# Kernel optimization log

Hardware: AMD Instinct MI355X
Metric: run time of the kernel (lower is better)

## Reference

```python
import jax, jax.numpy as jnp
import numpy as np


def setup_inputs() -> dict:
    key = jax.random.key(0)
    ks = jax.random.split(key, 6)
    B, T, S, E, D = 8, 128, 512, 512, 512  # batch, trg_len, src_len, enc_dim, trg_dim
    W_SCALE = 0.03  # small init to keep tanh unsaturated
    return {
        "hidden": jax.random.normal(ks[0], (B, T, D), jnp.float32),
        "encoder_outputs": jax.random.normal(ks[1], (B, S, E), jnp.float32),
        "encoder_mask": jnp.ones((B, S), jnp.float32),
        "W_attn": jax.random.normal(ks[2], (D, E + D), jnp.float32) * W_SCALE,
        "b_attn": jnp.zeros((D,), jnp.float32),
        "W_v": jax.random.normal(ks[3], (1, D), jnp.float32) * W_SCALE,
        "b_v": jnp.zeros((1,), jnp.float32),
        "W_out": jax.random.normal(ks[4], (D, E + D), jnp.float32) * W_SCALE,
    }


def masked_softmax(x, m, axis=-1):
    # faithful to repo: x*m, stable exp, e*m, normalize with eps
    x = x * m
    e_x = jnp.exp(x - jnp.max(x, axis=axis, keepdims=True))
    e_x = e_x * m
    return e_x / (jnp.sum(e_x, axis=axis, keepdims=True) + 1e-6)


def reference(hidden, encoder_outputs, encoder_mask, W_attn, b_attn, W_v, b_v, W_out):
    B, T, D = hidden.shape
    S = encoder_outputs.shape[1]
    # concat order in get_energy is (hidden_i, encoder_outputs), so split W_attn
    W_h = W_attn[:, :D]   # (D_out, trg_dim)
    W_e = W_attn[:, D:]   # (D_out, enc_dim)
    # Linear(concat) == h@W_h^T + e@W_e^T + b; vectorized over all (t, s) pairs
    hp = jnp.einsum('btd,kd->btk', hidden, W_h)            # (B,T,K)
    ep = jnp.einsum('bse,ke->bsk', encoder_outputs, W_e)   # (B,S,K)
    feat = jnp.tanh(hp[:, :, None, :] + ep[:, None, :, :] + b_attn)  # (B,T,S,K)
    energies = jnp.einsum('btsk,k->bts', feat, W_v[0]) + b_v[0]      # (B,T,S)
    # forward: energies * mask, then masked softmax
    m = encoder_mask[:, None, :]  # (B,1,S)
    energies = energies * m
    attn_weights = masked_softmax(energies, m, axis=-1)    # (B,T,S)
    weighted_context = jnp.einsum('bts,bse->bte', attn_weights, encoder_outputs)
    h_cat = jnp.concatenate([weighted_context, hidden], axis=-1)  # (B,T,E+D)
    h_tilde = jnp.tanh(jnp.einsum('btc,dc->btd', h_cat, W_out))   # (B,T,D)
    return h_tilde, weighted_context, attn_weights
```

## Files before the change

### kernel.cpp

```cpp
#include <hip/hip_runtime.h>
#include <hip/hip_bf16.h>
#include <math.h>

typedef unsigned short u16;
typedef unsigned int u32;
typedef __bf16 bf16x8 __attribute__((ext_vector_type(8)));
typedef float f32x4 __attribute__((ext_vector_type(4)));

#define OUT_WC   524288LL
#define OUT_ATTN 1048576LL
#define C2 2.8853900817779268f
#define LOG2E 1.4426950408889634f
#define LAS 40

__device__ inline u16 f2b(float f) {
    return (u16)((__float_as_uint(f) + 0x8000u) >> 16);
}
__device__ inline float b2f(u16 v) { return __uint_as_float(((u32)v) << 16); }
__device__ inline u32 pkcvt(float x, float y) {
    __hip_bfloat162 h = __float22bfloat162_rn(make_float2(x, y));
    return *(u32*)&h;
}
__device__ inline float tanh_fast(float x) {
    return 1.f - 2.f * __builtin_amdgcn_rcpf(__builtin_amdgcn_exp2f(C2 * x) + 1.f);
}

__global__ __launch_bounds__(256) void tobf(
    const float* __restrict__ enc, const float* __restrict__ hidden,
    const float* __restrict__ Wattn, const float* __restrict__ Wout,
    u16* __restrict__ dst)
{
    long long i = ((long long)blockIdx.x * 256 + threadIdx.x) * 8;
    const float* src; long long off;
    if (i < 2097152)      { src = enc;    off = i; }
    else if (i < 2621440) { src = hidden; off = i - 2097152; }
    else if (i < 3145728) { src = Wattn;  off = i - 2621440; }
    else                  { src = Wout;   off = i - 3145728; }
    float4 v0 = *(const float4*)(src + off);
    float4 v1 = *(const float4*)(src + off + 4);
    *(uint4*)(dst + i) = make_uint4(pkcvt(v0.x, v0.y), pkcvt(v0.z, v0.w),
                                    pkcvt(v1.x, v1.y), pkcvt(v1.z, v1.w));
}

__global__ __launch_bounds__(256) void proj(
    const u16* __restrict__ hidden_bf, const u16* __restrict__ enc_bf,
    const u16* __restrict__ Wattn_bf, const float* __restrict__ battn,
    const u16* __restrict__ Wout_bf,
    float* __restrict__ hp, u16* __restrict__ ept, float* __restrict__ hh)
{
    __shared__ u16 lA[64 * LAS];
    __shared__ u16 lB[64 * LAS];
    const int tid = threadIdx.x;
    const int wvi = tid >> 6, ln = tid & 63;
    const int wm = wvi >> 1, wn = wvi & 1;
    const int l16 = ln & 15, quad = ln >> 4;
    const int blk = blockIdx.x;
    int bx, by, zz = 0, lda, ldb, mode;
    const u16 *A, *B;
    if (blk < 512) {
        mode = 0;
        zz = blk >> 6; by = (blk >> 3) & 7; bx = blk & 7;
        A = Wattn_bf + 512; lda = 1024;
        B = enc_bf + (long long)zz * 262144; ldb = 512;
    } else if (blk < 640) {
        mode = 1;
        int i = blk - 512; by = i >> 3; bx = i & 7;
        A = hidden_bf; lda = 512;
        B = Wattn_bf; ldb = 1024;
    } else {
        mode = 2;
        int i = blk - 640; by = i >> 3; bx = i & 7;
        A = hidden_bf; lda = 512;
        B = Wout_bf + 512; ldb = 1024;
    }
    const int m0 = by * 64, n0 = bx * 64;
    const int srow = tid >> 2, skof = (tid & 3) * 8;
    const u16* Ap = A + (long long)(m0 + srow) * lda + skof;
    const u16* Bp = B + (long long)(n0 + srow) * ldb + skof;

    f32x4 acc00 = {0,0,0,0}, acc01 = {0,0,0,0}, acc10 = {0,0,0,0}, acc11 = {0,0,0,0};

    for (int k0 = 0; k0 < 512; k0 += 32) {
        uint4 av = *(const uint4*)(Ap + k0);
        uint4 bv = *(const uint4*)(Bp + k0);
        __syncthreads();
        *(uint4*)&lA[srow * LAS + skof] = av;
        *(uint4*)&lB[srow * LAS + skof] = bv;
        __syncthreads();
        bf16x8 a0 = *(const bf16x8*)&lA[(wm * 32      + l16) * LAS + quad * 8];
        bf16x8 a1 = *(const bf16x8*)&lA[(wm * 32 + 16 + l16) * LAS + quad * 8];
        bf16x8 b0 = *(const bf16x8*)&lB[(wn * 32      + l16) * LAS + quad * 8];
        bf16x8 b1 = *(const bf16x8*)&lB[(wn * 32 + 16 + l16) * LAS + quad * 8];
        acc00 = __builtin_amdgcn_mfma_f32_16x16x32_bf16(a0, b0, acc00, 0, 0, 0);
        acc01 = __builtin_amdgcn_mfma_f32_16x16x32_bf16(a0, b1, acc01, 0, 0, 0);
        acc10 = __builtin_amdgcn_mfma_f32_16x16x32_bf16(a1, b0, acc10, 0, 0, 0);
        acc11 = __builtin_amdgcn_mfma_f32_16x16x32_bf16(a1, b1, acc11, 0, 0, 0);
    }

    const f32x4* accs[4] = { &acc00, &acc01, &acc10, &acc11 };
    #pragma unroll
    for (int i = 0; i < 2; ++i) {
        #pragma unroll
        for (int j = 0; j < 2; ++j) {
            const f32x4& a = *accs[i * 2 + j];
            #pragma unroll
            for (int r = 0; r < 4; ++r) {
                int m = m0 + wm * 32 + i * 16 + quad * 4 + r;
                int n = n0 + wn * 32 + j * 16 + l16;
                float v = a[r];
                if (mode == 0)
                    ept[(long long)zz * 262144 + (long long)m * 512 + n] =
                        f2b(__builtin_amdgcn_exp2f(C2 * v));
                else if (mode == 1)
                    hp[(long long)m * 512 + n] = C2 * (v + battn[n]);
                else
                    hh[(long long)m * 512 + n] = v;
            }
        }
    }
}

__device__ inline float wred_sum(float v) {
    #pragma unroll
    for (int i = 32; i > 0; i >>= 1) v += __shfl_xor(v, i);
    return v;
}
__device__ inline float bred_sum8(float v, float* red, int tid) {
    v = wred_sum(v);
    __syncthreads();
    if ((tid & 63) == 0) red[tid >> 6] = v;
    __syncthreads();
    float s = 0.f;
    #pragma unroll
    for (int i = 0; i < 8; ++i) s += red[i];
    return s;
}
__device__ inline void bred2_max(float v0, float v1, float* red, int tid,
                                 float* o0, float* o1) {
    #pragma unroll
    for (int i = 32; i > 0; i >>= 1) {
        v0 = fmaxf(v0, __shfl_xor(v0, i));
        v1 = fmaxf(v1, __shfl_xor(v1, i));
    }
    __syncthreads();
    if ((tid & 63) == 0) { red[tid >> 6] = v0; red[8 + (tid >> 6)] = v1; }
    __syncthreads();
    float a0 = red[0], a1 = red[8];
    #pragma unroll
    for (int i = 1; i < 8; ++i) { a0 = fmaxf(a0, red[i]); a1 = fmaxf(a1, red[8 + i]); }
    *o0 = a0; *o1 = a1;
}
__device__ inline void bred2_sum(float v0, float v1, float* red, int tid,
                                 float* o0, float* o1) {
    #pragma unroll
    for (int i = 32; i > 0; i >>= 1) { v0 += __shfl_xor(v0, i); v1 += __shfl_xor(v1, i); }
    __syncthreads();
    if ((tid & 63) == 0) { red[tid >> 6] = v0; red[8 + (tid >> 6)] = v1; }
    __syncthreads();
    float a0 = 0.f, a1 = 0.f;
    #pragma unroll
    for (int i = 0; i < 8; ++i) { a0 += red[i]; a1 += red[8 + i]; }
    *o0 = a0; *o1 = a1;
}

__device__ inline void proc8(uint4 c, float4 hw, float* a0, float* a1) {
    u32 cc[4] = {c.x, c.y, c.z, c.w};
    #pragma unroll
    for (int i = 0; i < 4; ++i) {
        float xl = __uint_as_float(cc[i] << 16);
        float xh = __uint_as_float(cc[i] & 0xFFFF0000u);
        float rl0 = __builtin_amdgcn_rcpf(fmaf(hw.x, xl, 1.f));
        float rh0 = __builtin_amdgcn_rcpf(fmaf(hw.x, xh, 1.f));
        float rl1 = __builtin_amdgcn_rcpf(fmaf(hw.y, xl, 1.f));
        float rh1 = __builtin_amdgcn_rcpf(fmaf(hw.y, xh, 1.f));
        a0[2*i]   = fmaf(hw.z, rl0, a0[2*i]);
        a0[2*i+1] = fmaf(hw.z, rh0, a0[2*i+1]);
        a1[2*i]   = fmaf(hw.z, rl1, a1[2*i]);
        a1[2*i+1] = fmaf(hw.z, rh1, a1[2*i+1]);
    }
}

__global__ __launch_bounds__(512) void energies(
    const float* __restrict__ maskp, const float* __restrict__ hp,
    const u16* __restrict__ ept, const float* __restrict__ Wv,
    const float* __restrict__ bvp, const u16* __restrict__ enc_bf,
    float* __restrict__ attn, float* __restrict__ wc)
{
    __shared__ __align__(16) float4 hpw[512];
    __shared__ float pa[2][8][512];
    __shared__ __align__(16) float2 aL[512];
    __shared__ float red[16];
    const int tid = threadIdx.x;
    const int b = blockIdx.x >> 6;
    const int t0 = (blockIdx.x & 63) * 2;

    float w = Wv[tid];
    float h0 = hp[(long long)(b * 128 + t0) * 512 + tid];
    float h1 = hp[(long long)(b * 128 + t0 + 1) * 512 + tid];
    hpw[tid] = make_float4(__builtin_amdgcn_exp2f(h0), __builtin_amdgcn_exp2f(h1), w, 0.f);
    float sumWv = bred_sum8(w, red, tid);

    const int kg = tid >> 6, sl = tid & 63;
    const int s0 = sl * 8;
    const u16* eb = ept + (long long)b * 262144 + (kg * 64) * 512 + s0;
    const float4* hq = &hpw[kg * 64];

    float a0[8] = {0,0,0,0,0,0,0,0}, a1[8] = {0,0,0,0,0,0,0,0};
    uint4 c0 = *(const uint4*)(eb);
    uint4 c1 = *(const uint4*)(eb + 512);
    uint4 c2 = *(const uint4*)(eb + 1024);
    uint4 c3 = *(const uint4*)(eb + 1536);
    for (int kk = 0; kk < 60; kk += 4) {
        const u16* nb = eb + (kk + 4) * 512;
        uint4 n0 = *(const uint4*)(nb);
        uint4 n1 = *(const uint4*)(nb + 512);
        uint4 n2 = *(const uint4*)(nb + 1024);
        uint4 n3 = *(const uint4*)(nb + 1536);
        proc8(c0, hq[kk],     a0, a1);
        proc8(c1, hq[kk + 1], a0, a1);
        proc8(c2, hq[kk + 2], a0, a1);
        proc8(c3, hq[kk + 3], a0, a1);
        c0 = n0; c1 = n1; c2 = n2; c3 = n3;
    }
    proc8(c0, hq[60], a0, a1);
    proc8(c1, hq[61], a0, a1);
    proc8(c2, hq[62], a0, a1);
    proc8(c3, hq[63], a0, a1);

    *(float4*)&pa[0][kg][s0]     = make_float4(a0[0], a0[1], a0[2], a0[3]);
    *(float4*)&pa[0][kg][s0 + 4] = make_float4(a0[4], a0[5], a0[6], a0[7]);
    *(float4*)&pa[1][kg][s0]     = make_float4(a1[0], a1[1], a1[2], a1[3]);
    *(float4*)&pa[1][kg][s0 + 4] = make_float4(a1[4], a1[5], a1[6], a1[7]);
    __syncthreads();

    const int s = tid;
    float A0 = 0.f, A1 = 0.f;
    #pragma unroll
    for (int g = 0; g < 8; ++g) { A0 += pa[0][g][s]; A1 += pa[1][g][s]; }
    float mv = maskp[(long long)b * 512 + s];
    float bv0 = bvp[0];
    float r0 = (bv0 + sumWv - 2.f * A0) * mv; r0 *= mv;
    float r1 = (bv0 + sumWv - 2.f * A1) * mv; r1 *= mv;

    float mx0, mx1;
    bred2_max(r0, r1, red, tid, &mx0, &mx1);
    float ex0 = __builtin_amdgcn_exp2f((r0 - mx0) * LOG2E) * mv;
    float ex1 = __builtin_amdgcn_exp2f((r1 - mx1) * LOG2E) * mv;
    float sm0, sm1;
    bred2_sum(ex0, ex1, red, tid, &sm0, &sm1);
    float at0 = ex0 * (1.f / (sm0 + 1e-6f));
    float at1 = ex1 * (1.f / (sm1 + 1e-6f));
    attn[(long long)(b * 128 + t0) * 512 + s]     = at0;
    attn[(long long)(b * 128 + t0 + 1) * 512 + s] = at1;
    aL[s] = make_float2(at0, at1);
    __syncthreads();

    const u16* encb = enc_bf + (long long)b * 262144 + tid;
    const float4* aL4 = (const float4*)aL;
    float acc0 = 0.f, acc1 = 0.f;
    for (int ss = 0; ss < 512; ss += 8) {
        float ev[8];
        #pragma unroll
        for (int i = 0; i < 8; ++i) ev[i] = b2f(encb[(ss + i) * 512]);
        #pragma unroll
        for (int i = 0; i < 4; ++i) {
            float4 ap = aL4[(ss >> 1) + i];
            acc0 = fmaf(ap.x, ev[2*i],   acc0);
            acc1 = fmaf(ap.y, ev[2*i],   acc1);
            acc0 = fmaf(ap.z, ev[2*i+1], acc0);
            acc1 = fmaf(ap.w, ev[2*i+1], acc1);
        }
    }
    wc[(long long)(b * 128 + t0) * 512 + tid]     = acc0;
    wc[(long long)(b * 128 + t0 + 1) * 512 + tid] = acc1;
}

__global__ __launch_bounds__(256) void hout_k(
    const float* __restrict__ wc, const u16* __restrict__ Wout_bf,
    float* __restrict__ out)
{
    __shared__ u16 lA[32 * LAS];
    __shared__ u16 lB[64 * LAS];
    const int tid = threadIdx.x;
    const int wvi = tid >> 6, ln = tid & 63;
    const int l16 = ln & 15, quad = ln >> 4;
    const int msub = wvi & 1, npair = wvi >> 1;
    const int m0 = blockIdx.y * 32, n0 = blockIdx.x * 64;
    const int rowA = tid >> 3, kofA = (tid & 7) * 4;
    const int rowB = tid >> 2, kofB = (tid & 3) * 8;
    f32x4 acc0 = {0,0,0,0}, acc1 = {0,0,0,0};

    for (int k0 = 0; k0 < 512; k0 += 32) {
        float4 av = *(const float4*)(wc + (long long)(m0 + rowA) * 512 + k0 + kofA);
        uint4 bv = *(const uint4*)(Wout_bf + (long long)(n0 + rowB) * 1024 + k0 + kofB);
        __syncthreads();
        *(uint2*)&lA[rowA * LAS + kofA] = make_uint2(pkcvt(av.x, av.y), pkcvt(av.z, av.w));
        int kk = kofB ^ (((rowB >> 3) & 3) << 3);
        *(uint4*)&lB[rowB * LAS + kk] = bv;
        __syncthreads();
        bf16x8 a = *(const bf16x8*)&lA[(msub * 16 + l16) * LAS + quad * 8];
        int nr0 = npair * 32 + l16, nr1 = nr0 + 16;
        bf16x8 b0 = *(const bf16x8*)&lB[nr0 * LAS + (quad * 8 ^ (((nr0 >> 3) & 3) << 3))];
        bf16x8 b1 = *(const bf16x8*)&lB[nr1 * LAS + (quad * 8 ^ (((nr1 >> 3) & 3) << 3))];
        acc0 = __builtin_amdgcn_mfma_f32_16x16x32_bf16(a, b0, acc0, 0, 0, 0);
        acc1 = __builtin_amdgcn_mfma_f32_16x16x32_bf16(a, b1, acc1, 0, 0, 0);
    }
    #pragma unroll
    for (int j = 0; j < 2; ++j) {
        const f32x4& a = j ? acc1 : acc0;
        #pragma unroll
        for (int r = 0; r < 4; ++r) {
            int m = m0 + msub * 16 + quad * 4 + r;
            int n = n0 + npair * 32 + j * 16 + l16;
            long long idx = (long long)m * 512 + n;
            out[idx] = tanh_fast(a[r] + out[idx]);
        }
    }
}

extern "C" void kernel_launch(void* const* d_in, const int* in_sizes, int n_in,
                              void* d_out, int out_size, void* d_ws, size_t ws_size,
                              hipStream_t stream)
{
    const float* hidden = (const float*)d_in[0];
    const float* enc    = (const float*)d_in[1];
    const float* mask   = (const float*)d_in[2];
    const float* Wattn  = (const float*)d_in[3];
    const float* battn  = (const float*)d_in[4];
    const float* Wv     = (const float*)d_in[5];
    const float* bvp    = (const float*)d_in[6];
    const float* Wout   = (const float*)d_in[7];
    float* out = (float*)d_out;

    float* hp  = (float*)d_ws;
    u16*   ept = (u16*)((char*)d_ws + (2 << 20));
    u16*   bfp = (u16*)((char*)d_ws + (6 << 20));
    u16* enc_bf    = bfp;
    u16* hidden_bf = bfp + 2097152;
    u16* Wattn_bf  = bfp + 2621440;
    u16* Wout_bf   = bfp + 3145728;

    tobf<<<1792, 256, 0, stream>>>(enc, hidden, Wattn, Wout, bfp);
    proj<<<768, 256, 0, stream>>>(hidden_bf, enc_bf, Wattn_bf, battn, Wout_bf,
                                  hp, ept, out );
    energies<<<512, 512, 0, stream>>>(mask, hp, ept, Wv, bvp, enc_bf,
                                      out + OUT_ATTN, out + OUT_WC);
    hout_k<<<dim3(8, 32, 1), 256, 0, stream>>>(out + OUT_WC, Wout_bf, out);
}
```

Before: 148.9 us.

## Enlarge proj GEMM tiles to 128x128 with register prefetch of next K slice

The projection GEMM kernel now computes 128x128 output tiles per block instead of 64x64, with each wave holding a 4x4 grid of MFMA accumulators, and it loads the next K slice into registers while the current slice is being consumed. The larger tiles raise data reuse per LDS load and cut global traffic, and the prefetch is meant to hide global load latency. The trade-off is that the grid shrinks from 768 to 192 blocks, which is fewer than the CU count on MI355X, and register pressure per thread goes up. The LDS row padding also changes to 36.

```diff
diff --git a/kernel.cpp b/kernel.cpp
--- a/kernel.cpp
+++ b/kernel.cpp
@@ -12,6 +12,7 @@
 #define C2 2.8853900817779268f
 #define LOG2E 1.4426950408889634f
 #define LAS 40
+#define PLAS 36
 
 __device__ inline u16 f2b(float f) {
     return (u16)((__float_as_uint(f) + 0x8000u) >> 16);
@@ -48,66 +49,79 @@
     const u16* __restrict__ Wout_bf,
     float* __restrict__ hp, u16* __restrict__ ept, float* __restrict__ hh)
 {
-    __shared__ u16 lA[64 * LAS];
-    __shared__ u16 lB[64 * LAS];
+    __shared__ u16 lA[128 * PLAS];
+    __shared__ u16 lB[128 * PLAS];
     const int tid = threadIdx.x;
     const int wvi = tid >> 6, ln = tid & 63;
     const int wm = wvi >> 1, wn = wvi & 1;
     const int l16 = ln & 15, quad = ln >> 4;
     const int blk = blockIdx.x;
-    int bx, by, zz = 0, lda, ldb, mode;
+    int mode, bx, by, zz = 0, lda, ldb;
     const u16 *A, *B;
-    if (blk < 512) {
+    if (blk < 128) {
         mode = 0;
-        zz = blk >> 6; by = (blk >> 3) & 7; bx = blk & 7;
+        zz = blk >> 4; by = (blk >> 2) & 3; bx = blk & 3;
         A = Wattn_bf + 512; lda = 1024;
         B = enc_bf + (long long)zz * 262144; ldb = 512;
-    } else if (blk < 640) {
+    } else if (blk < 160) {
         mode = 1;
-        int i = blk - 512; by = i >> 3; bx = i & 7;
+        int i = blk - 128; by = i >> 2; bx = i & 3;
         A = hidden_bf; lda = 512;
         B = Wattn_bf; ldb = 1024;
     } else {
         mode = 2;
-        int i = blk - 640; by = i >> 3; bx = i & 7;
+        int i = blk - 160; by = i >> 2; bx = i & 3;
         A = hidden_bf; lda = 512;
         B = Wout_bf + 512; ldb = 1024;
     }
-    const int m0 = by * 64, n0 = bx * 64;
-    const int srow = tid >> 2, skof = (tid & 3) * 8;
-    const u16* Ap = A + (long long)(m0 + srow) * lda + skof;
-    const u16* Bp = B + (long long)(n0 + srow) * ldb + skof;
-
-    f32x4 acc00 = {0,0,0,0}, acc01 = {0,0,0,0}, acc10 = {0,0,0,0}, acc11 = {0,0,0,0};
+    const int m0 = by * 128, n0 = bx * 128;
+    const int sr = tid >> 2, sc = (tid & 3) * 8;
+    const u16* Ap0 = A + (long long)(m0 + sr) * lda + sc;
+    const u16* Ap1 = A + (long long)(m0 + sr + 64) * lda + sc;
+    const u16* Bp0 = B + (long long)(n0 + sr) * ldb + sc;
+    const u16* Bp1 = B + (long long)(n0 + sr + 64) * ldb + sc;
+
+    f32x4 acc[4][4] = {};
+    uint4 ra0 = *(const uint4*)(Ap0);
+    uint4 ra1 = *(const uint4*)(Ap1);
+    uint4 rb0 = *(const uint4*)(Bp0);
+    uint4 rb1 = *(const uint4*)(Bp1);
 
     for (int k0 = 0; k0 < 512; k0 += 32) {
-        uint4 av = *(const uint4*)(Ap + k0);
-        uint4 bv = *(const uint4*)(Bp + k0);
         __syncthreads();
-        *(uint4*)&lA[srow * LAS + skof] = av;
-        *(uint4*)&lB[srow * LAS + skof] = bv;
+        *(uint4*)&lA[sr * PLAS + sc]        = ra0;
+        *(uint4*)&lA[(sr + 64) * PLAS + sc] = ra1;
+        *(uint4*)&lB[sr * PLAS + sc]        = rb0;
+        *(uint4*)&lB[(sr + 64) * PLAS + sc] = rb1;
         __syncthreads();
-        bf16x8 a0 = *(const bf16x8*)&lA[(wm * 32      + l16) * LAS + quad * 8];
-        bf16x8 a1 = *(const bf16x8*)&lA[(wm * 32 + 16 + l16) * LAS + quad * 8];
-        bf16x8 b0 = *(const bf16x8*)&lB[(wn * 32      + l16) * LAS + quad * 8];
-        bf16x8 b1 = *(const bf16x8*)&lB[(wn * 32 + 16 + l16) * LAS + quad * 8];
-        acc00 = __builtin_amdgcn_mfma_f32_16x16x32_bf16(a0, b0, acc00, 0, 0, 0);
-        acc01 = __builtin_amdgcn_mfma_f32_16x16x32_bf16(a0, b1, acc01, 0, 0, 0);
-        acc10 = __builtin_amdgcn_mfma_f32_16x16x32_bf16(a1, b0, acc10, 0, 0, 0);
-        acc11 = __builtin_amdgcn_mfma_f32_16x16x32_bf16(a1, b1, acc11, 0, 0, 0);
-    }
-
-    const f32x4* accs[4] = { &acc00, &acc01, &acc10, &acc11 };
-    #pragma unroll
-    for (int i = 0; i < 2; ++i) {
-        #pragma unroll
-        for (int j = 0; j < 2; ++j) {
-            const f32x4& a = *accs[i * 2 + j];
+        if (k0 + 32 < 512) {
+            ra0 = *(const uint4*)(Ap0 + k0 + 32);
+            ra1 = *(const uint4*)(Ap1 + k0 + 32);
+            rb0 = *(const uint4*)(Bp0 + k0 + 32);
+            rb1 = *(const uint4*)(Bp1 + k0 + 32);
+        }
+        bf16x8 af[4], bfr[4];
+        #pragma unroll
+        for (int i = 0; i < 4; ++i) {
+            af[i]  = *(const bf16x8*)&lA[(wm * 64 + i * 16 + l16) * PLAS + quad * 8];
+            bfr[i] = *(const bf16x8*)&lB[(wn * 64 + i * 16 + l16) * PLAS + quad * 8];
+        }
+        #pragma unroll
+        for (int i = 0; i < 4; ++i)
+            #pragma unroll
+            for (int j = 0; j < 4; ++j)
+                acc[i][j] = __builtin_amdgcn_mfma_f32_16x16x32_bf16(af[i], bfr[j], acc[i][j], 0, 0, 0);
+    }
+
+    #pragma unroll
+    for (int i = 0; i < 4; ++i) {
+        #pragma unroll
+        for (int j = 0; j < 4; ++j) {
             #pragma unroll
             for (int r = 0; r < 4; ++r) {
-                int m = m0 + wm * 32 + i * 16 + quad * 4 + r;
-                int n = n0 + wn * 32 + j * 16 + l16;
-                float v = a[r];
+                int m = m0 + wm * 64 + i * 16 + quad * 4 + r;
+                int n = n0 + wn * 64 + j * 16 + l16;
+                float v = acc[i][j][r];
                 if (mode == 0)
                     ept[(long long)zz * 262144 + (long long)m * 512 + n] =
                         f2b(__builtin_amdgcn_exp2f(C2 * v));
@@ -341,7 +355,7 @@
     u16* Wout_bf   = bfp + 3145728;
 
     tobf<<<1792, 256, 0, stream>>>(enc, hidden, Wattn, Wout, bfp);
-    proj<<<768, 256, 0, stream>>>(hidden_bf, enc_bf, Wattn_bf, battn, Wout_bf,
+    proj<<<192, 256, 0, stream>>>(hidden_bf, enc_bf, Wattn_bf, battn, Wout_bf,
                                   hp, ept, out );
     energies<<<512, 512, 0, stream>>>(mask, hp, ept, Wv, bvp, enc_bf,
                                       out + OUT_ATTN, out + OUT_WC);
```

New measurement: 157.3 us. 5.7% more time.

## Fuse output projection into energies kernel using transposed bf16 Wout

Applied to the files above, without the earlier changes.

Removes the separate hout_k MFMA kernel. The energies kernel now finishes the h_tilde GEMV itself: it keeps the weighted context in shared memory and multiplies it by a transposed bf16 copy of the context half of W_out. The conversion kernel now builds that transposed copy through a shared-memory tile transpose and packs the hidden half of W_out contiguously. This saves one launch and the re-read of wc, but each energies block now streams the whole 512x512 weight with scalar FMAs rather than using MFMA tiles, and that work sits at the tail of an already heavy kernel.

```diff
diff --git a/kernel.cpp b/kernel.cpp
--- a/kernel.cpp
+++ b/kernel.cpp
@@ -13,6 +13,12 @@
 #define LOG2E 1.4426950408889634f
 #define LAS 40
 
+#define P_ENC    0LL
+#define P_HID    2097152LL
+#define P_WATTN  2621440LL
+#define P_WOUTR  3145728LL
+#define P_WOUTTL 3407872LL
+
 __device__ inline u16 f2b(float f) {
     return (u16)((__float_as_uint(f) + 0x8000u) >> 16);
 }
@@ -30,22 +36,52 @@
     const float* __restrict__ Wattn, const float* __restrict__ Wout,
     u16* __restrict__ dst)
 {
-    long long i = ((long long)blockIdx.x * 256 + threadIdx.x) * 8;
-    const float* src; long long off;
-    if (i < 2097152)      { src = enc;    off = i; }
-    else if (i < 2621440) { src = hidden; off = i - 2097152; }
-    else if (i < 3145728) { src = Wattn;  off = i - 2621440; }
-    else                  { src = Wout;   off = i - 3145728; }
-    float4 v0 = *(const float4*)(src + off);
-    float4 v1 = *(const float4*)(src + off + 4);
-    *(uint4*)(dst + i) = make_uint4(pkcvt(v0.x, v0.y), pkcvt(v0.z, v0.w),
-                                    pkcvt(v1.x, v1.y), pkcvt(v1.z, v1.w));
+    const int tid = threadIdx.x;
+    if (blockIdx.x < 1664) {
+        long long i = ((long long)blockIdx.x * 256 + tid) * 8;
+        const float* src;
+        if (i < 2097152)      src = enc + i;
+        else if (i < 2621440) src = hidden + (i - 2097152);
+        else if (i < 3145728) src = Wattn + (i - 2621440);
+        else {
+            long long j = i - 3145728;
+            src = Wout + ((j >> 9) << 10) + 512 + (j & 511);
+        }
+        float4 v0 = *(const float4*)src;
+        float4 v1 = *(const float4*)(src + 4);
+        *(uint4*)(dst + i) = make_uint4(pkcvt(v0.x, v0.y), pkcvt(v0.z, v0.w),
+                                        pkcvt(v1.x, v1.y), pkcvt(v1.z, v1.w));
+    } else {
+        __shared__ u32 lt[64 * 66];
+        int tt = blockIdx.x - 1664;
+        int n0 = (tt >> 3) * 64, d0 = (tt & 7) * 64;
+        int r = tid >> 2, c = (tid & 3) * 16;
+        const float* sp = Wout + (long long)(n0 + r) * 1024 + d0 + c;
+        #pragma unroll
+        for (int q = 0; q < 4; ++q) {
+            float4 v = *(const float4*)(sp + q * 4);
+            lt[r * 66 + c + q * 4 + 0] = f2b(v.x);
+            lt[r * 66 + c + q * 4 + 1] = f2b(v.y);
+            lt[r * 66 + c + q * 4 + 2] = f2b(v.z);
+            lt[r * 66 + c + q * 4 + 3] = f2b(v.w);
+        }
+        __syncthreads();
+        int dr = tid >> 2, nc = (tid & 3) * 16;
+        u32 o[8];
+        #pragma unroll
+        for (int q = 0; q < 8; ++q) {
+            u32 lo = lt[(nc + 2 * q) * 66 + dr];
+            u32 hi = lt[(nc + 2 * q + 1) * 66 + dr];
+            o[q] = lo | (hi << 16);
+        }
+        u16* dp = dst + P_WOUTTL + (long long)(d0 + dr) * 512 + n0 + nc;
+        *(uint4*)dp       = make_uint4(o[0], o[1], o[2], o[3]);
+        *(uint4*)(dp + 8) = make_uint4(o[4], o[5], o[6], o[7]);
+    }
 }
 
 __global__ __launch_bounds__(256) void proj(
-    const u16* __restrict__ hidden_bf, const u16* __restrict__ enc_bf,
-    const u16* __restrict__ Wattn_bf, const float* __restrict__ battn,
-    const u16* __restrict__ Wout_bf,
+    const u16* __restrict__ pool, const float* __restrict__ battn,
     float* __restrict__ hp, u16* __restrict__ ept, float* __restrict__ hh)
 {
     __shared__ u16 lA[64 * LAS];
@@ -60,18 +96,18 @@
     if (blk < 512) {
         mode = 0;
         zz = blk >> 6; by = (blk >> 3) & 7; bx = blk & 7;
-        A = Wattn_bf + 512; lda = 1024;
-        B = enc_bf + (long long)zz * 262144; ldb = 512;
+        A = pool + P_WATTN + 512; lda = 1024;
+        B = pool + P_ENC + (long long)zz * 262144; ldb = 512;
     } else if (blk < 640) {
         mode = 1;
         int i = blk - 512; by = i >> 3; bx = i & 7;
-        A = hidden_bf; lda = 512;
-        B = Wattn_bf; ldb = 1024;
+        A = pool + P_HID; lda = 512;
+        B = pool + P_WATTN; ldb = 1024;
     } else {
         mode = 2;
         int i = blk - 640; by = i >> 3; bx = i & 7;
-        A = hidden_bf; lda = 512;
-        B = Wout_bf + 512; ldb = 1024;
+        A = pool + P_HID; lda = 512;
+        B = pool + P_WOUTR; ldb = 512;
     }
     const int m0 = by * 64, n0 = bx * 64;
     const int srow = tid >> 2, skof = (tid & 3) * 8;
@@ -183,16 +219,19 @@
 __global__ __launch_bounds__(512) void energies(
     const float* __restrict__ maskp, const float* __restrict__ hp,
     const u16* __restrict__ ept, const float* __restrict__ Wv,
-    const float* __restrict__ bvp, const u16* __restrict__ enc_bf,
-    float* __restrict__ attn, float* __restrict__ wc)
+    const float* __restrict__ bvp, const u16* __restrict__ pool,
+    float* __restrict__ out)
 {
     __shared__ __align__(16) float4 hpw[512];
     __shared__ float pa[2][8][512];
     __shared__ __align__(16) float2 aL[512];
+    __shared__ __align__(16) float2 wcL[512];
     __shared__ float red[16];
     const int tid = threadIdx.x;
     const int b = blockIdx.x >> 6;
     const int t0 = (blockIdx.x & 63) * 2;
+    const u16* enc_bf = pool + P_ENC;
+    const u16* woutT  = pool + P_WOUTTL;
 
     float w = Wv[tid];
     float h0 = hp[(long long)(b * 128 + t0) * 512 + tid];
@@ -250,71 +289,55 @@
     bred2_sum(ex0, ex1, red, tid, &sm0, &sm1);
     float at0 = ex0 * (1.f / (sm0 + 1e-6f));
     float at1 = ex1 * (1.f / (sm1 + 1e-6f));
-    attn[(long long)(b * 128 + t0) * 512 + s]     = at0;
-    attn[(long long)(b * 128 + t0 + 1) * 512 + s] = at1;
+    out[OUT_ATTN + (long long)(b * 128 + t0) * 512 + s]     = at0;
+    out[OUT_ATTN + (long long)(b * 128 + t0 + 1) * 512 + s] = at1;
     aL[s] = make_float2(at0, at1);
     __syncthreads();
 
-    const u16* encb = enc_bf + (long long)b * 262144 + tid;
-    const float4* aL4 = (const float4*)aL;
-    float acc0 = 0.f, acc1 = 0.f;
-    for (int ss = 0; ss < 512; ss += 8) {
-        float ev[8];
-        #pragma unroll
-        for (int i = 0; i < 8; ++i) ev[i] = b2f(encb[(ss + i) * 512]);
-        #pragma unroll
-        for (int i = 0; i < 4; ++i) {
-            float4 ap = aL4[(ss >> 1) + i];
-            acc0 = fmaf(ap.x, ev[2*i],   acc0);
-            acc1 = fmaf(ap.y, ev[2*i],   acc1);
-            acc0 = fmaf(ap.z, ev[2*i+1], acc0);
-            acc1 = fmaf(ap.w, ev[2*i+1], acc1);
-        }
-    }
-    wc[(long long)(b * 128 + t0) * 512 + tid]     = acc0;
-    wc[(long long)(b * 128 + t0 + 1) * 512 + tid] = acc1;
-}
-
-__global__ __launch_bounds__(256) void hout_k(
-    const float* __restrict__ wc, const u16* __restrict__ Wout_bf,
-    float* __restrict__ out)
-{
-    __shared__ u16 lA[32 * LAS];
-    __shared__ u16 lB[64 * LAS];
-    const int tid = threadIdx.x;
-    const int wvi = tid >> 6, ln = tid & 63;
-    const int l16 = ln & 15, quad = ln >> 4;
-    const int msub = wvi & 1, npair = wvi >> 1;
-    const int m0 = blockIdx.y * 32, n0 = blockIdx.x * 64;
-    const int rowA = tid >> 3, kofA = (tid & 7) * 4;
-    const int rowB = tid >> 2, kofB = (tid & 3) * 8;
-    f32x4 acc0 = {0,0,0,0}, acc1 = {0,0,0,0};
-
-    for (int k0 = 0; k0 < 512; k0 += 32) {
-        float4 av = *(const float4*)(wc + (long long)(m0 + rowA) * 512 + k0 + kofA);
-        uint4 bv = *(const uint4*)(Wout_bf + (long long)(n0 + rowB) * 1024 + k0 + kofB);
-        __syncthreads();
-        *(uint2*)&lA[rowA * LAS + kofA] = make_uint2(pkcvt(av.x, av.y), pkcvt(av.z, av.w));
-        int kk = kofB ^ (((rowB >> 3) & 3) << 3);
-        *(uint4*)&lB[rowB * LAS + kk] = bv;
-        __syncthreads();
-        bf16x8 a = *(const bf16x8*)&lA[(msub * 16 + l16) * LAS + quad * 8];
-        int nr0 = npair * 32 + l16, nr1 = nr0 + 16;
-        bf16x8 b0 = *(const bf16x8*)&lB[nr0 * LAS + (quad * 8 ^ (((nr0 >> 3) & 3) << 3))];
-        bf16x8 b1 = *(const bf16x8*)&lB[nr1 * LAS + (quad * 8 ^ (((nr1 >> 3) & 3) << 3))];
-        acc0 = __builtin_amdgcn_mfma_f32_16x16x32_bf16(a, b0, acc0, 0, 0, 0);
-        acc1 = __builtin_amdgcn_mfma_f32_16x16x32_bf16(a, b1, acc1, 0, 0, 0);
-    }
-    #pragma unroll
-    for (int j = 0; j < 2; ++j) {
-        const f32x4& a = j ? acc1 : acc0;
-        #pragma unroll
-        for (int r = 0; r < 4; ++r) {
-            int m = m0 + msub * 16 + quad * 4 + r;
-            int n = n0 + npair * 32 + j * 16 + l16;
-            long long idx = (long long)m * 512 + n;
-            out[idx] = tanh_fast(a[r] + out[idx]);
-        }
+    {
+        const u16* encb = enc_bf + (long long)b * 262144 + tid;
+        const float4* aL4 = (const float4*)aL;
+        float acc0 = 0.f, acc1 = 0.f;
+        for (int ss = 0; ss < 512; ss += 8) {
+            float ev[8];
+            #pragma unroll
+            for (int i = 0; i < 8; ++i) ev[i] = b2f(encb[(ss + i) * 512]);
+            #pragma unroll
+            for (int i = 0; i < 4; ++i) {
+                float4 ap = aL4[(ss >> 1) + i];
+                acc0 = fmaf(ap.x, ev[2*i],   acc0);
+                acc1 = fmaf(ap.y, ev[2*i],   acc1);
+                acc0 = fmaf(ap.z, ev[2*i+1], acc0);
+                acc1 = fmaf(ap.w, ev[2*i+1], acc1);
+            }
+        }
+        out[OUT_WC + (long long)(b * 128 + t0) * 512 + tid]     = acc0;
+        out[OUT_WC + (long long)(b * 128 + t0 + 1) * 512 + tid] = acc1;
+        wcL[tid] = make_float2(acc0, acc1);
+    }
+    __syncthreads();
+
+    {
+        const u16* wt = woutT + tid;
+        const float4* wL4 = (const float4*)wcL;
+        float acc0 = 0.f, acc1 = 0.f;
+        for (int dd = 0; dd < 512; dd += 8) {
+            float wv[8];
+            #pragma unroll
+            for (int i = 0; i < 8; ++i) wv[i] = b2f(wt[(dd + i) * 512]);
+            #pragma unroll
+            for (int i = 0; i < 4; ++i) {
+                float4 cp = wL4[(dd >> 1) + i];
+                acc0 = fmaf(cp.x, wv[2*i],   acc0);
+                acc1 = fmaf(cp.y, wv[2*i],   acc1);
+                acc0 = fmaf(cp.z, wv[2*i+1], acc0);
+                acc1 = fmaf(cp.w, wv[2*i+1], acc1);
+            }
+        }
+        long long o0 = (long long)(b * 128 + t0) * 512 + tid;
+        long long o1 = (long long)(b * 128 + t0 + 1) * 512 + tid;
+        out[o0] = tanh_fast(acc0 + out[o0]);
+        out[o1] = tanh_fast(acc1 + out[o1]);
     }
 }
 
@@ -334,16 +357,9 @@
 
     float* hp  = (float*)d_ws;
     u16*   ept = (u16*)((char*)d_ws + (2 << 20));
-    u16*   bfp = (u16*)((char*)d_ws + (6 << 20));
-    u16* enc_bf    = bfp;
-    u16* hidden_bf = bfp + 2097152;
-    u16* Wattn_bf  = bfp + 2621440;
-    u16* Wout_bf   = bfp + 3145728;
-
-    tobf<<<1792, 256, 0, stream>>>(enc, hidden, Wattn, Wout, bfp);
-    proj<<<768, 256, 0, stream>>>(hidden_bf, enc_bf, Wattn_bf, battn, Wout_bf,
-                                  hp, ept, out );
-    energies<<<512, 512, 0, stream>>>(mask, hp, ept, Wv, bvp, enc_bf,
-                                      out + OUT_ATTN, out + OUT_WC);
-    hout_k<<<dim3(8, 32, 1), 256, 0, stream>>>(out + OUT_WC, Wout_bf, out);
-}
+    u16*   pool = (u16*)((char*)d_ws + (6 << 20));
+
+    tobf<<<1728, 256, 0, stream>>>(enc, hidden, Wattn, Wout, pool);
+    proj<<<768, 256, 0, stream>>>(pool, battn, hp, ept, out );
+    energies<<<512, 512, 0, stream>>>(mask, hp, ept, Wv, bvp, pool, out);
+}
```

New measurement: 153.5 us. 3.1% more time.
